# Kernel optimization log

Measured on AMD Instinct MI355X. Metric: run time of the kernel, lower is better.

The kernel has to match this reference:

```python
import jax, jax.numpy as jnp
import numpy as np

N = 50000          # nodes
E = 200000         # edges
IN_C = 16          # in_channels
HID_C = 32         # hidden_channels (NNConv output)
EDGE_D = 8         # edge_attr_dim
OUT_C = 32         # out_channels (gnn output)
MLP_H = 128        # q_head hidden_dim
N_ACT = 32         # num_actions


def setup_inputs() -> dict:
    key = jax.random.key(0)
    ks = jax.random.split(key, 16)
    s = 0.05
    inp = {
        "x": jax.random.normal(ks[0], (N, IN_C), jnp.float32),
        "edge_src": jax.random.randint(ks[1], (E,), 0, N, jnp.int32),
        "edge_dst": jax.random.randint(ks[2], (E,), 0, N, jnp.int32),
        "edge_attr": jax.random.normal(ks[3], (E, EDGE_D), jnp.float32),
        # edge_nn: Linear(EDGE_D, IN_C*HID_C) + ReLU
        "We": jax.random.normal(ks[4], (EDGE_D, IN_C * HID_C), jnp.float32) * s,
        "be": jnp.zeros((IN_C * HID_C,), jnp.float32),
        # NNConv root weight + bias
        "Wroot": jax.random.normal(ks[5], (IN_C, HID_C), jnp.float32) * s,
        "bconv": jnp.zeros((HID_C,), jnp.float32),
        # LayerNorm over hidden_channels
        "gamma": jnp.ones((HID_C,), jnp.float32),
        "beta": jnp.zeros((HID_C,), jnp.float32),
        # gnn.lin: Linear(HID_C, OUT_C)
        "Wlin": jax.random.normal(ks[6], (HID_C, OUT_C), jnp.float32) * s,
        "blin": jnp.zeros((OUT_C,), jnp.float32),
        # q_head: Linear(OUT_C, MLP_H) -> ReLU -> Linear(MLP_H, N_ACT)
        "Wq1": jax.random.normal(ks[7], (OUT_C, MLP_H), jnp.float32) * s,
        "bq1": jnp.zeros((MLP_H,), jnp.float32),
        "Wq2": jax.random.normal(ks[8], (MLP_H, N_ACT), jnp.float32) * s,
        "bq2": jnp.zeros((N_ACT,), jnp.float32),
    }
    return inp


def reference(x, edge_src, edge_dst, edge_attr,
              We, be, Wroot, bconv, gamma, beta,
              Wlin, blin, Wq1, bq1, Wq2, bq2):
    # --- NNConv: per-edge weight from edge MLP ---
    w_e = jax.nn.relu(edge_attr @ We + be)              # [E, IN_C*HID_C]
    w_e = w_e.reshape(E, IN_C, HID_C)
    x_j = x[edge_src]                                    # gather source feats [E, IN_C]
    msg = jnp.einsum('ei,eih->eh', x_j, w_e)             # per-edge matmul [E, HID_C]
    agg = jax.ops.segment_sum(msg, edge_dst, num_segments=N)  # scatter-add [N, HID_C]
    h = agg + x @ Wroot + bconv                          # root + bias
    # --- LayerNorm + ReLU + Linear ---
    mu = jnp.mean(h, axis=-1, keepdims=True)
    var = jnp.mean((h - mu) ** 2, axis=-1, keepdims=True)
    h = (h - mu) / jnp.sqrt(var + 1e-5) * gamma + beta
    h = jax.nn.relu(h)
    feat = h @ Wlin + blin                               # [N, OUT_C]
    # --- q_head MLP ---
    q = jax.nn.relu(feat @ Wq1 + bq1) @ Wq2 + bq2        # [N, N_ACT]
    return q.reshape(-1, N_ACT)
```

## Files before the change

kernel.cpp:

```cpp
#include <hip/hip_runtime.h>

#define NN   50000
#define NE   200000
#define INC  16
#define HIDC 32
#define EDGED 8
#define OUTC 32
#define MLPH 128
#define NACT 32

#define NPART 196
#define NQUAD (NE / 2)
#define EDGE_GRID 784

typedef float floatx4 __attribute__((ext_vector_type(4)));

__global__ __launch_bounds__(256) void hist_slot_kernel(const int* __restrict__ edst,
                                                        int* __restrict__ deg,
                                                        int* __restrict__ slot) {
    int e = blockIdx.x * blockDim.x + threadIdx.x;
    if (e < NE) slot[e] = atomicAdd(&deg[edst[e]], 1);
}

__global__ __launch_bounds__(256) void partial_kernel(const int* __restrict__ deg,
                                                      int* __restrict__ partials) {
    __shared__ int sm[256];
    int t = threadIdx.x, i = blockIdx.x * 256 + t;
    sm[t] = (i < NN) ? deg[i] : 0;
    __syncthreads();
    #pragma unroll
    for (int off = 128; off > 0; off >>= 1) {
        if (t < off) sm[t] += sm[t + off];
        __syncthreads();
    }
    if (t == 0) partials[blockIdx.x] = sm[0];
}

__global__ __launch_bounds__(256) void rowoff2_kernel(const int* __restrict__ deg,
                                                      const int* __restrict__ partials,
                                                      int* __restrict__ row_off) {
    __shared__ int sp[NPART];
    __shared__ int sm[256];
    int t = threadIdx.x, bid = blockIdx.x;
    if (t < NPART) sp[t] = partials[t];
    __syncthreads();
    int base = 0;
    for (int i = 0; i < bid; ++i) base += sp[i];

    int i = bid * 256 + t;
    int d = (i < NN) ? deg[i] : 0;
    sm[t] = d;
    __syncthreads();
    for (int off = 1; off < 256; off <<= 1) {
        int v = (t >= off) ? sm[t - off] : 0;
        __syncthreads();
        sm[t] += v;
        __syncthreads();
    }
    int excl = sm[t] - d + base;
    if (i < NN) {
        row_off[i] = excl;
        if (i == NN - 1) row_off[NN] = excl + d;
    }
}

__global__ __launch_bounds__(256, 4) void edge_q2_kernel(
    const float* __restrict__ x,
    const int*   __restrict__ esrc,
    const int*   __restrict__ edst,
    const float* __restrict__ ea,
    const float* __restrict__ We,
    const float* __restrict__ be,
    const int*   __restrict__ row_off,
    const int*   __restrict__ slot,
    float*       __restrict__ sorted_msg)
{
    __shared__ float sWe2[4 * 1032];
    __shared__ float sbe2[4 * 132];
    int t = threadIdx.x;
    for (int idx = t; idx < 4 * 1032; idx += 256) {
        int l = idx / 1032, r = idx - l * 1032;
        float v = 0.f;
        if (r < 1024) {
            int d = r & 7, icc = r >> 3;
            int i = icc >> 3, cc = icc & 7;
            int h = ((cc & 4) << 2) + l * 4 + (cc & 3);
            v = We[d * 512 + i * 32 + h];
        }
        sWe2[idx] = v;
    }
    for (int idx = t; idx < 4 * 132; idx += 256) {
        int l = idx / 132, r = idx - l * 132;
        float v = 0.f;
        if (r < 128) {
            int i = r >> 3, cc = r & 7;
            int h = ((cc & 4) << 2) + l * 4 + (cc & 3);
            v = be[i * 32 + h];
        }
        sbe2[idx] = v;
    }
    __syncthreads();

    int l = t & 3;
    const float* wl = sWe2 + l * 1032;
    const float* bl = sbe2 + l * 132;

    for (int q = blockIdx.x * 64 + (t >> 2); q < NQUAD; q += EDGE_GRID * 64) {
        int e0 = q, e1 = q + 100000;
        int s0 = esrc[e0], s1 = esrc[e1];
        int p0 = row_off[edst[e0]] + slot[e0];
        int p1 = row_off[edst[e1]] + slot[e1];

        float ea0[8], ea1[8];
        {
            const float4* p;
            float4 a, b;
            p = reinterpret_cast<const float4*>(ea) + (size_t)e0 * 2; a = p[0]; b = p[1];
            ea0[0]=a.x; ea0[1]=a.y; ea0[2]=a.z; ea0[3]=a.w; ea0[4]=b.x; ea0[5]=b.y; ea0[6]=b.z; ea0[7]=b.w;
            p = reinterpret_cast<const float4*>(ea) + (size_t)e1 * 2; a = p[0]; b = p[1];
            ea1[0]=a.x; ea1[1]=a.y; ea1[2]=a.z; ea1[3]=a.w; ea1[4]=b.x; ea1[5]=b.y; ea1[6]=b.z; ea1[7]=b.w;
        }

        float m0[8], m1[8];
        #pragma unroll
        for (int c = 0; c < 8; ++c) { m0[c]=0.f; m1[c]=0.f; }

        const float4* xp0 = reinterpret_cast<const float4*>(x) + (size_t)s0 * 4;
        const float4* xp1 = reinterpret_cast<const float4*>(x) + (size_t)s1 * 4;

        for (int i4 = 0; i4 < 4; ++i4) {
            float4 xv0 = xp0[i4], xv1 = xp1[i4];
            float xs0[4] = {xv0.x, xv0.y, xv0.z, xv0.w};
            float xs1[4] = {xv1.x, xv1.y, xv1.z, xv1.w};
            const float* wb4 = wl + i4 * 256;
            const float* bb4 = bl + i4 * 32;
            #pragma unroll
            for (int ii = 0; ii < 4; ++ii) {
                const float* wbase = wb4 + ii * 64;
                const float* bbase = bb4 + ii * 8;
                float xi0 = xs0[ii], xi1 = xs1[ii];
                #pragma unroll
                for (int cc = 0; cc < 8; ++cc) {
                    const float* wr = wbase + cc * 8;
                    float bv = bbase[cc];
                    float w0 = bv, w1 = bv;
                    #pragma unroll
                    for (int d = 0; d < 8; ++d) {
                        float wd = wr[d];
                        w0 = fmaf(ea0[d], wd, w0);
                        w1 = fmaf(ea1[d], wd, w1);
                    }
                    w0 = fmaxf(w0, 0.f); w1 = fmaxf(w1, 0.f);
                    m0[cc] = fmaf(xi0, w0, m0[cc]);
                    m1[cc] = fmaf(xi1, w1, m1[cc]);
                }
            }
        }

        floatx4* o;
        floatx4 v;
        o = reinterpret_cast<floatx4*>(sorted_msg + (size_t)p0 * 32 + l * 4);
        v = (floatx4){m0[0], m0[1], m0[2], m0[3]}; __builtin_nontemporal_store(v, o);
        v = (floatx4){m0[4], m0[5], m0[6], m0[7]}; __builtin_nontemporal_store(v, o + 4);
        o = reinterpret_cast<floatx4*>(sorted_msg + (size_t)p1 * 32 + l * 4);
        v = (floatx4){m1[0], m1[1], m1[2], m1[3]}; __builtin_nontemporal_store(v, o);
        v = (floatx4){m1[4], m1[5], m1[6], m1[7]}; __builtin_nontemporal_store(v, o + 4);
    }
}

__global__ __launch_bounds__(64, 1) void node_fused_kernel(
    const float* __restrict__ x,
    const float* __restrict__ sorted_msg,
    const int*   __restrict__ row_off,
    const float* __restrict__ Wroot,
    const float* __restrict__ bconv,
    const float* __restrict__ gamma,
    const float* __restrict__ beta,
    const float* __restrict__ Wlin,
    const float* __restrict__ blin,
    const float* __restrict__ Wq1,
    const float* __restrict__ bq1,
    const float* __restrict__ Wq2,
    const float* __restrict__ bq2,
    float* __restrict__ out)
{
    __shared__ float sw1[4 * 1032];
    int t = threadIdx.x;
    for (int w = t; w < 4096; w += 64) {
        int k = w >> 7, m = w & 127, l = m >> 5, j = m & 31;
        sw1[l * 1032 + k * 32 + j] = Wq1[w];
    }
    __syncthreads();

    int gid = blockIdx.x * 64 + t;
    int p = gid >> 2;
    int l = gid & 3;
    if (p >= NN / 2) return;
    int n0 = p * 2, n1 = p * 2 + 1;
    int o1 = l * 4;
    int o2 = 16 + l * 4;

    float h0[8], h1[8];
    {
        float4 a = *reinterpret_cast<const float4*>(bconv + o1);
        float4 b = *reinterpret_cast<const float4*>(bconv + o2);
        h0[0]=a.x; h0[1]=a.y; h0[2]=a.z; h0[3]=a.w;
        h0[4]=b.x; h0[5]=b.y; h0[6]=b.z; h0[7]=b.w;
        #pragma unroll
        for (int c = 0; c < 8; ++c) h1[c] = h0[c];
    }

    int r0 = row_off[n0], r1 = row_off[n1], r2 = row_off[n1 + 1];
    for (int k = r0; k < r1; ++k) {
        const float* row = sorted_msg + (size_t)k * 32;
        float4 a = *reinterpret_cast<const float4*>(row + o1);
        float4 b = *reinterpret_cast<const float4*>(row + o2);
        h0[0]+=a.x; h0[1]+=a.y; h0[2]+=a.z; h0[3]+=a.w;
        h0[4]+=b.x; h0[5]+=b.y; h0[6]+=b.z; h0[7]+=b.w;
    }
    for (int k = r1; k < r2; ++k) {
        const float* row = sorted_msg + (size_t)k * 32;
        float4 a = *reinterpret_cast<const float4*>(row + o1);
        float4 b = *reinterpret_cast<const float4*>(row + o2);
        h1[0]+=a.x; h1[1]+=a.y; h1[2]+=a.z; h1[3]+=a.w;
        h1[4]+=b.x; h1[5]+=b.y; h1[6]+=b.z; h1[7]+=b.w;
    }

    {
        const float4* xa = reinterpret_cast<const float4*>(x) + (size_t)n0 * 4;
        const float4* xb = reinterpret_cast<const float4*>(x) + (size_t)n1 * 4;
        #pragma unroll
        for (int i4 = 0; i4 < 4; ++i4) {
            float4 xv0 = xa[i4], xv1 = xb[i4];
            float xs0[4] = {xv0.x, xv0.y, xv0.z, xv0.w};
            float xs1[4] = {xv1.x, xv1.y, xv1.z, xv1.w};
            #pragma unroll
            for (int ii = 0; ii < 4; ++ii) {
                const float* wr = Wroot + (i4 * 4 + ii) * HIDC;
                float4 a = *reinterpret_cast<const float4*>(wr + o1);
                float4 b = *reinterpret_cast<const float4*>(wr + o2);
                float xi0 = xs0[ii], xi1 = xs1[ii];
                h0[0]=fmaf(xi0,a.x,h0[0]); h0[1]=fmaf(xi0,a.y,h0[1]);
                h0[2]=fmaf(xi0,a.z,h0[2]); h0[3]=fmaf(xi0,a.w,h0[3]);
                h0[4]=fmaf(xi0,b.x,h0[4]); h0[5]=fmaf(xi0,b.y,h0[5]);
                h0[6]=fmaf(xi0,b.z,h0[6]); h0[7]=fmaf(xi0,b.w,h0[7]);
                h1[0]=fmaf(xi1,a.x,h1[0]); h1[1]=fmaf(xi1,a.y,h1[1]);
                h1[2]=fmaf(xi1,a.z,h1[2]); h1[3]=fmaf(xi1,a.w,h1[3]);
                h1[4]=fmaf(xi1,b.x,h1[4]); h1[5]=fmaf(xi1,b.y,h1[5]);
                h1[6]=fmaf(xi1,b.z,h1[6]); h1[7]=fmaf(xi1,b.w,h1[7]);
            }
        }
    }

    float s0 = ((h0[0]+h0[1])+(h0[2]+h0[3])) + ((h0[4]+h0[5])+(h0[6]+h0[7]));
    float s1 = ((h1[0]+h1[1])+(h1[2]+h1[3])) + ((h1[4]+h1[5])+(h1[6]+h1[7]));
    s0 += __shfl_xor(s0, 1); s0 += __shfl_xor(s0, 2);
    s1 += __shfl_xor(s1, 1); s1 += __shfl_xor(s1, 2);
    float mu0 = s0 * (1.f / HIDC), mu1 = s1 * (1.f / HIDC);
    float v0 = 0.f, v1 = 0.f;
    #pragma unroll
    for (int c = 0; c < 8; ++c) {
        float d0 = h0[c] - mu0; v0 = fmaf(d0, d0, v0);
        float d1 = h1[c] - mu1; v1 = fmaf(d1, d1, v1);
    }
    v0 += __shfl_xor(v0, 1); v0 += __shfl_xor(v0, 2);
    v1 += __shfl_xor(v1, 1); v1 += __shfl_xor(v1, 2);
    float rs0 = rsqrtf(v0 * (1.f / HIDC) + 1e-5f);
    float rs1 = rsqrtf(v1 * (1.f / HIDC) + 1e-5f);
    {
        float4 g0 = *reinterpret_cast<const float4*>(gamma + o1);
        float4 g1 = *reinterpret_cast<const float4*>(gamma + o2);
        float4 b0 = *reinterpret_cast<const float4*>(beta + o1);
        float4 b1 = *reinterpret_cast<const float4*>(beta + o2);
        float gs[8] = {g0.x,g0.y,g0.z,g0.w,g1.x,g1.y,g1.z,g1.w};
        float bs[8] = {b0.x,b0.y,b0.z,b0.w,b1.x,b1.y,b1.z,b1.w};
        #pragma unroll
        for (int c = 0; c < 8; ++c) {
            h0[c] = fmaxf(fmaf((h0[c] - mu0) * rs0, gs[c], bs[c]), 0.f);
            h1[c] = fmaxf(fmaf((h1[c] - mu1) * rs1, gs[c], bs[c]), 0.f);
        }
    }

    float fA[8], fB[8];
    {
        float4 a = *reinterpret_cast<const float4*>(blin + o1);
        float4 b = *reinterpret_cast<const float4*>(blin + o2);
        fA[0]=a.x; fA[1]=a.y; fA[2]=a.z; fA[3]=a.w;
        fA[4]=b.x; fA[5]=b.y; fA[6]=b.z; fA[7]=b.w;
        #pragma unroll
        for (int c = 0; c < 8; ++c) fB[c] = fA[c];
    }
    #pragma unroll
    for (int srcl = 0; srcl < 4; ++srcl) {
        #pragma unroll
        for (int c = 0; c < 8; ++c) {
            float hv0 = __shfl(h0[c], srcl, 4);
            float hv1 = __shfl(h1[c], srcl, 4);
            int k = ((c & 4) << 2) + srcl * 4 + (c & 3);
            const float* wr = Wlin + k * OUTC;
            float4 a = *reinterpret_cast<const float4*>(wr + o1);
            float4 b = *reinterpret_cast<const float4*>(wr + o2);
            fA[0]=fmaf(hv0,a.x,fA[0]); fA[1]=fmaf(hv0,a.y,fA[1]);
            fA[2]=fmaf(hv0,a.z,fA[2]); fA[3]=fmaf(hv0,a.w,fA[3]);
            fA[4]=fmaf(hv0,b.x,fA[4]); fA[5]=fmaf(hv0,b.y,fA[5]);
            fA[6]=fmaf(hv0,b.z,fA[6]); fA[7]=fmaf(hv0,b.w,fA[7]);
            fB[0]=fmaf(hv1,a.x,fB[0]); fB[1]=fmaf(hv1,a.y,fB[1]);
            fB[2]=fmaf(hv1,a.z,fB[2]); fB[3]=fmaf(hv1,a.w,fB[3]);
            fB[4]=fmaf(hv1,b.x,fB[4]); fB[5]=fmaf(hv1,b.y,fB[5]);
            fB[6]=fmaf(hv1,b.z,fB[6]); fB[7]=fmaf(hv1,b.w,fB[7]);
        }
    }

    float f0[OUTC], f1[OUTC];
    #pragma unroll
    for (int srcl = 0; srcl < 4; ++srcl) {
        #pragma unroll
        for (int c = 0; c < 8; ++c) {
            int k = ((c & 4) << 2) + srcl * 4 + (c & 3);
            f0[k] = __shfl(fA[c], srcl, 4);
            f1[k] = __shfl(fB[c], srcl, 4);
        }
    }

    float acc0[32], acc1[32];
    {
        const float4* b4 = reinterpret_cast<const float4*>(bq1 + l * 32);
        #pragma unroll
        for (int j4 = 0; j4 < 8; ++j4) {
            float4 b = b4[j4];
            acc0[j4*4+0]=b.x; acc0[j4*4+1]=b.y; acc0[j4*4+2]=b.z; acc0[j4*4+3]=b.w;
            acc1[j4*4+0]=b.x; acc1[j4*4+1]=b.y; acc1[j4*4+2]=b.z; acc1[j4*4+3]=b.w;
        }
    }
    const float* w1 = sw1 + l * 1032;
    #pragma unroll
    for (int k = 0; k < 32; ++k) {
        float fk0 = f0[k], fk1 = f1[k];
        const float* wr = w1 + k * 32;
        #pragma unroll
        for (int j = 0; j < 32; ++j) {
            float wj = wr[j];
            acc0[j] = fmaf(fk0, wj, acc0[j]);
            acc1[j] = fmaf(fk1, wj, acc1[j]);
        }
    }
    #pragma unroll
    for (int j = 0; j < 32; ++j) {
        acc0[j] = fmaxf(acc0[j], 0.f);
        acc1[j] = fmaxf(acc1[j], 0.f);
    }

    float q0[8], q1[8];
    {
        const float4* b4 = reinterpret_cast<const float4*>(bq2 + l * 8);
        float4 a = b4[0], b = b4[1];
        q0[0]=a.x; q0[1]=a.y; q0[2]=a.z; q0[3]=a.w;
        q0[4]=b.x; q0[5]=b.y; q0[6]=b.z; q0[7]=b.w;
        #pragma unroll
        for (int c = 0; c < 8; ++c) q1[c] = q0[c];
    }
    #pragma unroll
    for (int srcl = 0; srcl < 4; ++srcl) {
        #pragma unroll
        for (int j = 0; j < 32; ++j) {
            float a0 = __shfl(acc0[j], srcl, 4);
            float a1 = __shfl(acc1[j], srcl, 4);
            int m = srcl * 32 + j;
            const float4* w2 = reinterpret_cast<const float4*>(Wq2 + m * NACT + l * 8);
            float4 wa = w2[0], wb = w2[1];
            q0[0]=fmaf(a0,wa.x,q0[0]); q0[1]=fmaf(a0,wa.y,q0[1]);
            q0[2]=fmaf(a0,wa.z,q0[2]); q0[3]=fmaf(a0,wa.w,q0[3]);
            q0[4]=fmaf(a0,wb.x,q0[4]); q0[5]=fmaf(a0,wb.y,q0[5]);
            q0[6]=fmaf(a0,wb.z,q0[6]); q0[7]=fmaf(a0,wb.w,q0[7]);
            q1[0]=fmaf(a1,wa.x,q1[0]); q1[1]=fmaf(a1,wa.y,q1[1]);
            q1[2]=fmaf(a1,wa.z,q1[2]); q1[3]=fmaf(a1,wa.w,q1[3]);
            q1[4]=fmaf(a1,wb.x,q1[4]); q1[5]=fmaf(a1,wb.y,q1[5]);
            q1[6]=fmaf(a1,wb.z,q1[6]); q1[7]=fmaf(a1,wb.w,q1[7]);
        }
    }

    float4* o;
    o = reinterpret_cast<float4*>(out + (size_t)n0 * NACT + l * 8);
    o[0] = make_float4(q0[0], q0[1], q0[2], q0[3]);
    o[1] = make_float4(q0[4], q0[5], q0[6], q0[7]);
    o = reinterpret_cast<float4*>(out + (size_t)n1 * NACT + l * 8);
    o[0] = make_float4(q1[0], q1[1], q1[2], q1[3]);
    o[1] = make_float4(q1[4], q1[5], q1[6], q1[7]);
}

extern "C" void kernel_launch(void* const* d_in, const int* in_sizes, int n_in,
                              void* d_out, int out_size, void* d_ws, size_t ws_size,
                              hipStream_t stream) {
    const float* x     = (const float*)d_in[0];
    const int*   esrc  = (const int*)d_in[1];
    const int*   edst  = (const int*)d_in[2];
    const float* ea    = (const float*)d_in[3];
    const float* We    = (const float*)d_in[4];
    const float* be    = (const float*)d_in[5];
    const float* Wroot = (const float*)d_in[6];
    const float* bconv = (const float*)d_in[7];
    const float* gamma = (const float*)d_in[8];
    const float* beta  = (const float*)d_in[9];
    const float* Wlin  = (const float*)d_in[10];
    const float* blin  = (const float*)d_in[11];
    const float* Wq1   = (const float*)d_in[12];
    const float* bq1   = (const float*)d_in[13];
    const float* Wq2   = (const float*)d_in[14];
    const float* bq2   = (const float*)d_in[15];
    float* out = (float*)d_out;

    char* ws = (char*)d_ws;
    int*   deg        = (int*)(ws + 0);
    int*   slot       = (int*)(ws + 200704);
    int*   row_off    = (int*)(ws + 1001472);
    int*   partials   = (int*)(ws + 1203200);
    float* sorted_msg = (float*)(ws + 1204224);

    hipMemsetAsync(deg, 0, 200704, stream);

    hist_slot_kernel<<<(NE + 255) / 256, 256, 0, stream>>>(edst, deg, slot);
    partial_kernel<<<NPART, 256, 0, stream>>>(deg, partials);
    rowoff2_kernel<<<NPART, 256, 0, stream>>>(deg, partials, row_off);
    edge_q2_kernel<<<EDGE_GRID, 256, 0, stream>>>(
        x, esrc, edst, ea, We, be, row_off, slot, sorted_msg);
    node_fused_kernel<<<(NN / 2 * 4 + 63) / 64, 64, 0, stream>>>(
        x, sorted_msg, row_off, Wroot, bconv, gamma, beta,
        Wlin, blin, Wq1, bq1, Wq2, bq2, out);
}
```

Measured before the change: 103.6 us.

## Process one edge per thread group instead of two-edge grid-stride loop

```diff
diff --git a/kernel.cpp b/kernel.cpp
--- a/kernel.cpp
+++ b/kernel.cpp
@@ -10,8 +10,6 @@
 #define NACT 32
 
 #define NPART 196
-#define NQUAD (NE / 2)
-#define EDGE_GRID 784
 
 typedef float floatx4 __attribute__((ext_vector_type(4)));
 
@@ -64,7 +62,7 @@
     }
 }
 
-__global__ __launch_bounds__(256, 4) void edge_q2_kernel(
+__global__ __launch_bounds__(256, 4) void edge_q1_kernel(
     const float* __restrict__ x,
     const int*   __restrict__ esrc,
     const int*   __restrict__ edst,
@@ -101,71 +99,57 @@
     }
     __syncthreads();
 
-    int l = t & 3;
+    int gid = blockIdx.x * 256 + t;
+    int e = gid >> 2;
+    int l = gid & 3;
+    if (e >= NE) return;
+
+    int src = esrc[e];
+    int pos = row_off[edst[e]] + slot[e];
+
+    float ea8[8];
+    {
+        const float4* p = reinterpret_cast<const float4*>(ea) + (size_t)e * 2;
+        float4 a = p[0], b = p[1];
+        ea8[0]=a.x; ea8[1]=a.y; ea8[2]=a.z; ea8[3]=a.w;
+        ea8[4]=b.x; ea8[5]=b.y; ea8[6]=b.z; ea8[7]=b.w;
+    }
+
+    float m[8];
+    #pragma unroll
+    for (int c = 0; c < 8; ++c) m[c] = 0.f;
+
     const float* wl = sWe2 + l * 1032;
     const float* bl = sbe2 + l * 132;
-
-    for (int q = blockIdx.x * 64 + (t >> 2); q < NQUAD; q += EDGE_GRID * 64) {
-        int e0 = q, e1 = q + 100000;
-        int s0 = esrc[e0], s1 = esrc[e1];
-        int p0 = row_off[edst[e0]] + slot[e0];
-        int p1 = row_off[edst[e1]] + slot[e1];
-
-        float ea0[8], ea1[8];
-        {
-            const float4* p;
-            float4 a, b;
-            p = reinterpret_cast<const float4*>(ea) + (size_t)e0 * 2; a = p[0]; b = p[1];
-            ea0[0]=a.x; ea0[1]=a.y; ea0[2]=a.z; ea0[3]=a.w; ea0[4]=b.x; ea0[5]=b.y; ea0[6]=b.z; ea0[7]=b.w;
-            p = reinterpret_cast<const float4*>(ea) + (size_t)e1 * 2; a = p[0]; b = p[1];
-            ea1[0]=a.x; ea1[1]=a.y; ea1[2]=a.z; ea1[3]=a.w; ea1[4]=b.x; ea1[5]=b.y; ea1[6]=b.z; ea1[7]=b.w;
-        }
-
-        float m0[8], m1[8];
-        #pragma unroll
-        for (int c = 0; c < 8; ++c) { m0[c]=0.f; m1[c]=0.f; }
-
-        const float4* xp0 = reinterpret_cast<const float4*>(x) + (size_t)s0 * 4;
-        const float4* xp1 = reinterpret_cast<const float4*>(x) + (size_t)s1 * 4;
-
-        for (int i4 = 0; i4 < 4; ++i4) {
-            float4 xv0 = xp0[i4], xv1 = xp1[i4];
-            float xs0[4] = {xv0.x, xv0.y, xv0.z, xv0.w};
-            float xs1[4] = {xv1.x, xv1.y, xv1.z, xv1.w};
-            const float* wb4 = wl + i4 * 256;
-            const float* bb4 = bl + i4 * 32;
+    const float4* xp = reinterpret_cast<const float4*>(x) + (size_t)src * 4;
+
+    for (int i4 = 0; i4 < 4; ++i4) {
+        float4 xv = xp[i4];
+        float xs[4] = {xv.x, xv.y, xv.z, xv.w};
+        const float* wb4 = wl + i4 * 256;
+        const float* bb4 = bl + i4 * 32;
+        #pragma unroll
+        for (int ii = 0; ii < 4; ++ii) {
+            const float* wbase = wb4 + ii * 64;
+            const float* bbase = bb4 + ii * 8;
+            float xi = xs[ii];
             #pragma unroll
-            for (int ii = 0; ii < 4; ++ii) {
-                const float* wbase = wb4 + ii * 64;
-                const float* bbase = bb4 + ii * 8;
-                float xi0 = xs0[ii], xi1 = xs1[ii];
+            for (int cc = 0; cc < 8; ++cc) {
+                const float* wr = wbase + cc * 8;
+                float w = bbase[cc];
                 #pragma unroll
-                for (int cc = 0; cc < 8; ++cc) {
-                    const float* wr = wbase + cc * 8;
-                    float bv = bbase[cc];
-                    float w0 = bv, w1 = bv;
-                    #pragma unroll
-                    for (int d = 0; d < 8; ++d) {
-                        float wd = wr[d];
-                        w0 = fmaf(ea0[d], wd, w0);
-                        w1 = fmaf(ea1[d], wd, w1);
-                    }
-                    w0 = fmaxf(w0, 0.f); w1 = fmaxf(w1, 0.f);
-                    m0[cc] = fmaf(xi0, w0, m0[cc]);
-                    m1[cc] = fmaf(xi1, w1, m1[cc]);
-                }
+                for (int d = 0; d < 8; ++d)
+                    w = fmaf(ea8[d], wr[d], w);
+                w = fmaxf(w, 0.f);
+                m[cc] = fmaf(xi, w, m[cc]);
             }
         }
-
-        floatx4* o;
-        floatx4 v;
-        o = reinterpret_cast<floatx4*>(sorted_msg + (size_t)p0 * 32 + l * 4);
-        v = (floatx4){m0[0], m0[1], m0[2], m0[3]}; __builtin_nontemporal_store(v, o);
-        v = (floatx4){m0[4], m0[5], m0[6], m0[7]}; __builtin_nontemporal_store(v, o + 4);
-        o = reinterpret_cast<floatx4*>(sorted_msg + (size_t)p1 * 32 + l * 4);
-        v = (floatx4){m1[0], m1[1], m1[2], m1[3]}; __builtin_nontemporal_store(v, o);
-        v = (floatx4){m1[4], m1[5], m1[6], m1[7]}; __builtin_nontemporal_store(v, o + 4);
-    }
+    }
+
+    floatx4* o = reinterpret_cast<floatx4*>(sorted_msg + (size_t)pos * 32 + l * 4);
+    floatx4 v;
+    v = (floatx4){m[0], m[1], m[2], m[3]}; __builtin_nontemporal_store(v, o);
+    v = (floatx4){m[4], m[5], m[6], m[7]}; __builtin_nontemporal_store(v, o + 4);
 }
 
 __global__ __launch_bounds__(64, 1) void node_fused_kernel(
@@ -421,7 +405,7 @@
     hist_slot_kernel<<<(NE + 255) / 256, 256, 0, stream>>>(edst, deg, slot);
     partial_kernel<<<NPART, 256, 0, stream>>>(deg, partials);
     rowoff2_kernel<<<NPART, 256, 0, stream>>>(deg, partials, row_off);
-    edge_q2_kernel<<<EDGE_GRID, 256, 0, stream>>>(
+    edge_q1_kernel<<<(NE * 4 + 255) / 256, 256, 0, stream>>>(
         x, esrc, edst, ea, We, be, row_off, slot, sorted_msg);
     node_fused_kernel<<<(NN / 2 * 4 + 63) / 64, 64, 0, stream>>>(
         x, sorted_msg, row_off, Wroot, bconv, gamma, beta,
```

Measured after the change: 107.0 us. 3.3% more time.
